# Optimization experiments

Hardware: AMD Instinct MI355X
Metric: run time of the kernel (lower is better)

## Reference

```python
import jax, jax.numpy as jnp
import numpy as np
from jax import lax

# FPN anchor layout: 800x800 image, 3 anchors/loc, strides 4,8,16,32,64
LEVEL_ANCHORS = [120000, 30000, 7500, 1875, 507]
PRE_NMS_TOP_N = 1000   # per level (test mode)
POST_NMS_TOP_N = 1000
NMS_THRESH = 0.7
MIN_SIZE = 1e-3


def setup_inputs() -> dict:
    key = jax.random.key(0)
    k1, k2, k3, k4 = jax.random.split(key, 4)
    A = sum(LEVEL_ANCHORS)
    bs = 2
    predicts = jax.random.normal(k1, (bs, A, 4), jnp.float32) * 0.1
    objectness = jax.random.normal(k2, (bs, A, 1), jnp.float32)
    cxy = jax.random.uniform(k3, (A, 2), jnp.float32, 0.0, 800.0)
    wh = jax.random.uniform(k4, (A, 2), jnp.float32, 16.0, 128.0)
    anchors = jnp.concatenate([cxy - 0.5 * wh, cxy + 0.5 * wh], axis=-1)
    valid_size = jnp.full((bs, 2), 800.0, jnp.float32)  # (w, h) per image
    return {"predicts": predicts, "objectness": objectness,
            "anchors": anchors, "valid_size": valid_size}


def _decode(predicts, anchors):
    # BoxCoder.decoder with weights [1,1,1,1]
    awh = anchors[:, 2:] - anchors[:, :2]          # [A,2]
    axy = anchors[:, :2] + 0.5 * awh               # [A,2]
    xy = axy + predicts[..., :2] * awh             # [bs,A,2] center
    wh = jnp.exp(predicts[..., 2:]) * awh          # [bs,A,2]
    x1y1 = xy - 0.5 * wh
    return jnp.concatenate([x1y1, x1y1 + wh], axis=-1)  # [bs,A,4]


def _per_level_topk_idx(scores):
    # scores: [bs, A] -> concat of per-level top-k indices (global anchor ids)
    idx_list, offset = [], 0
    for n in LEVEL_ANCHORS:
        k = min(PRE_NMS_TOP_N, n)
        _, top = lax.top_k(scores[:, offset:offset + n], k)
        idx_list.append(top + offset)
        offset += n
    return jnp.concatenate(idx_list, axis=1)  # [bs, K]


def _nms_keep(boxes, valid, thresh):
    # boxes sorted by score desc; returns boolean keep mask (sequential NMS)
    x1, y1, x2, y2 = boxes[:, 0], boxes[:, 1], boxes[:, 2], boxes[:, 3]
    area = (x2 - x1) * (y2 - y1)
    xx1 = jnp.maximum(x1[:, None], x1[None, :])
    yy1 = jnp.maximum(y1[:, None], y1[None, :])
    xx2 = jnp.minimum(x2[:, None], x2[None, :])
    yy2 = jnp.minimum(y2[:, None], y2[None, :])
    inter = jnp.maximum(xx2 - xx1, 0.0) * jnp.maximum(yy2 - yy1, 0.0)
    iou = inter / (area[:, None] + area[None, :] - inter + 1e-9)
    sup = iou > thresh                                   # [N,N]
    N = boxes.shape[0]
    ar = jnp.arange(N)

    def body(i, keep):
        suppressed = jnp.any((ar < i) & keep & sup[i])
        return keep.at[i].set(keep[i] & ~suppressed)

    return lax.fori_loop(0, N, body, valid)


def _filter_image(boxes, scores, lvls, wh):
    # boxes [K,4], scores [K], lvls [K] int, wh [2]=(w,h)
    w, h = wh[0], wh[1]
    x1 = jnp.clip(boxes[:, 0], 0.0, w)
    y1 = jnp.clip(boxes[:, 1], 0.0, h)
    x2 = jnp.clip(boxes[:, 2], 0.0, w)
    y2 = jnp.clip(boxes[:, 3], 0.0, h)
    boxes = jnp.stack([x1, y1, x2, y2], axis=-1)
    valid = (x2 - x1 > MIN_SIZE) & (y2 - y1 > MIN_SIZE)
    s = jnp.where(valid, scores, -jnp.inf)
    order = jnp.argsort(-s)
    boxes, s, lvls, valid = boxes[order], s[order], lvls[order], valid[order]
    # batched_nms: offset each level into a disjoint coordinate range
    max_coord = lax.stop_gradient(jnp.max(boxes)) + 1.0
    off = lvls.astype(boxes.dtype) * max_coord
    keep = _nms_keep(lax.stop_gradient(boxes) + off[:, None], valid, NMS_THRESH)
    # take first POST_NMS_TOP_N kept (boxes are score-sorted)
    rank = jnp.cumsum(keep) - 1
    slot = jnp.where(keep & (rank < POST_NMS_TOP_N), rank, POST_NMS_TOP_N)
    out_b = jnp.zeros((POST_NMS_TOP_N + 1, 4), boxes.dtype).at[slot].set(boxes)[:POST_NMS_TOP_N]
    out_s = jnp.zeros((POST_NMS_TOP_N + 1,), s.dtype).at[slot].set(
        jnp.where(keep, s, 0.0))[:POST_NMS_TOP_N]
    return out_b, out_s


def reference(predicts, objectness, anchors, valid_size):
    bs = predicts.shape[0]
    proposals = _decode(predicts, anchors)            # [bs,A,4]
    scores = objectness[..., 0]                       # [bs,A]
    idx = _per_level_topk_idx(scores)                 # [bs,K]
    bidx = jnp.arange(bs)[:, None]
    boxes = proposals[bidx, idx]                      # [bs,K,4]
    sc = scores[bidx, idx]                            # [bs,K]
    levels_all = jnp.concatenate(
        [jnp.full((n,), i, jnp.int32) for i, n in enumerate(LEVEL_ANCHORS)])
    lvl = levels_all[idx]                             # [bs,K]
    final_boxes, final_scores = jax.vmap(_filter_image)(boxes, sc, lvl, valid_size)
    return final_boxes, final_scores
```

## Files before the change

kernel.cpp:

```cpp
#include <hip/hip_runtime.h>

typedef unsigned int u32;
typedef unsigned long long u64;

#define A_TOT    159882
#define BS       2
#define KTOP     1000
#define CAND_CAP 4096
#define HB       4096
#define ABLK     4096
#define NBH      40
#define EPT      16

static const size_t HIST12_OFF   = 0;
static const size_t CUT_OFF      = 131072;
static const size_t CCNT_OFF     = 131104;
static const size_t MAXC_OFF     = 131136;
static const size_t NV_OFF       = 131144;
static const size_t CHUNKANY_OFF = 131200;
static const size_t ZERO_END     = 132480;
static const size_t CAND_OFF     = 132480;
static const size_t LKEY2_OFF    = 394624;
static const size_t LBOX_OFF     = 476544;
static const size_t LSC_OFF      = 640384;
static const size_t RANK_OFF     = 681344;
static const size_t MASK_OFF     = 759168;

__device__ __forceinline__ int level_of(int a) {
  if (a < 120000) return 0;
  if (a < 150000) return 1;
  if (a < 157500) return 2;
  if (a < 159375) return 3;
  return 4;
}

__device__ __forceinline__ u32 dkey(float s) {
  u32 b = __float_as_uint(s);
  return (b & 0x80000000u) ? b : (~b & 0x7FFFFFFFu);
}
__device__ __forceinline__ float dkey_inv(u32 d) {
  u32 b = (d & 0x80000000u) ? d : (~d & 0x7FFFFFFFu);
  return __uint_as_float(b);
}

__device__ __forceinline__ void decode_clip(const float* __restrict__ pred,
                                            const float* __restrict__ anch,
                                            const float* __restrict__ vs,
                                            int b, int a,
                                            float& x1c, float& y1c, float& x2c, float& y2c,
                                            bool& valid) {
  const float* pp = pred + ((size_t)b * A_TOT + (size_t)a) * 4;
  const float* aa = anch + (size_t)a * 4;
  float ax1 = aa[0], ay1 = aa[1], ax2 = aa[2], ay2 = aa[3];
  float px = pp[0], py = pp[1], pw = pp[2], ph = pp[3];
  float aw  = __fsub_rn(ax2, ax1);
  float ah  = __fsub_rn(ay2, ay1);
  float acx = __fadd_rn(ax1, __fmul_rn(0.5f, aw));
  float acy = __fadd_rn(ay1, __fmul_rn(0.5f, ah));
  float cx  = __fadd_rn(acx, __fmul_rn(px, aw));
  float cy  = __fadd_rn(acy, __fmul_rn(py, ah));
  float w   = __fmul_rn(expf(pw), aw);
  float h   = __fmul_rn(expf(ph), ah);
  float x1  = __fsub_rn(cx, __fmul_rn(0.5f, w));
  float y1  = __fsub_rn(cy, __fmul_rn(0.5f, h));
  float x2  = __fadd_rn(x1, w);
  float y2  = __fadd_rn(y1, h);
  float Wv = vs[b * 2 + 0], Hv = vs[b * 2 + 1];
  x1c = fminf(fmaxf(x1, 0.0f), Wv);
  y1c = fminf(fmaxf(y1, 0.0f), Hv);
  x2c = fminf(fmaxf(x2, 0.0f), Wv);
  y2c = fminf(fmaxf(y2, 0.0f), Hv);
  valid = (__fsub_rn(x2c, x1c) > 0.001f) && (__fsub_rn(y2c, y1c) > 0.001f);
}

__device__ __forceinline__ void bitonic_u64(u64* arr, int N, int t, int nt) {
// ... 31 lines not shown
        bool sw = up ? (a > b2) : (a < b2);
        if (sw) { v[0] = b2; v[1] = a; }
      } else if (j <= 64) {
        int dl = j >> 1;
        bool up = (((2 * tid) & k) == 0);
        bool low = ((tid & dl) == 0);
        bool keepmin = (low == up);
#pragma unroll
        for (int e = 0; e < 2; ++e) {
          u64 o = shfl_xor_u64(v[e], dl);
          v[e] = keepmin ? (v[e] < o ? v[e] : o) : (v[e] > o ? v[e] : o);
        }
      } else {
        u64* B = bufs[cur]; cur ^= 1;
        B[2 * tid] = v[0]; B[2 * tid + 1] = v[1];
        __syncthreads();
#pragma unroll
        for (int e = 0; e < 2; ++e) {
          int i = 2 * tid + e, p = i ^ j;
          u64 o = B[p];
          bool up = ((i & k) == 0);
          bool keepmin = ((i < p) == up);
          v[e] = keepmin ? (v[e] < o ? v[e] : o) : (v[e] > o ? v[e] : o);
        }
      }
    }
  }
  u64* B = bufs[cur];
  B[2 * tid] = v[0]; B[2 * tid + 1] = v[1];
  __syncthreads();
  return B;
}

__global__ void k_zero(char* __restrict__ ws) {
  size_t i = (size_t)blockIdx.x * blockDim.x + threadIdx.x;
  if (i * 4 < ZERO_END) ((u32*)ws)[i] = 0u;
}

__global__ void k_hist12(const float* __restrict__ obj, char* __restrict__ ws) {
  __shared__ u32 h[2 * HB];
  int tid = threadIdx.x;
  int b = blockIdx.x / NBH, loc = blockIdx.x % NBH;
  int start = loc * ABLK;
  int l0 = level_of(start);
  if (l0 >= 4) return;
  for (int i = tid; i < 2 * HB; i += 256) h[i] = 0u;
  __syncthreads();
  for (int it = 0; it < EPT; ++it) {
    int a = start + it * 256 + tid;
    if (a < A_TOT) {
      int l = level_of(a);
      if (l < 4) {
        u32 d = dkey(obj[(size_t)b * A_TOT + a]);
        atomicAdd(&h[(u32)(l - l0) * HB + (d >> 20)], 1u);
      }
    }
  }
  __syncthreads();
  int lend = level_of(min(start + ABLK - 1, A_TOT - 1));
  int nseg = ((l0 + 1 <= lend) && (l0 + 1 < 4)) ? 2 : 1;
  for (int s = 0; s < nseg; ++s) {
    u32* gh = (u32*)(ws + HIST12_OFF) + (size_t)(b * 4 + l0 + s) * HB;
    for (int i = tid; i < HB; i += 256) {
      u32 v = h[s * HB + i];
      if (v) atomicAdd(&gh[i], v);
    }
  }
}

__global__ void k_compactsel(const float* __restrict__ obj, char* __restrict__ ws) {
  __shared__ u32 scan[256];
  __shared__ u32 cutv[2];
  __shared__ u32 lcnt[2], gbase[2];
  int tid = threadIdx.x, lane = tid & 63;
  int b = blockIdx.x / NBH, loc = blockIdx.x % NBH;
  int start = loc * ABLK;
  int l0 = level_of(start);
  if (l0 >= 4) return;
  int lend = level_of(min(start + ABLK - 1, A_TOT - 1));
  int nseg = ((l0 + 1 <= lend) && (l0 + 1 < 4)) ? 2 : 1;
  if (tid < 2) lcnt[tid] = 0;
  for (int s = 0; s < nseg; ++s) {
    int seg = b * 4 + l0 + s;
    const u32* gh = (const u32*)(ws + HIST12_OFF) + (size_t)seg * HB;
    u32 vals[16]; u32 acc = 0;
    for (int q = 0; q < 16; ++q) { vals[q] = gh[tid * 16 + q]; acc += vals[q]; }
    __syncthreads();
    scan[tid] = acc; __syncthreads();
    for (int d = 1; d < 256; d <<= 1) {
      u32 x = (tid >= d) ? scan[tid - d] : 0u; __syncthreads();
      scan[tid] += x; __syncthreads();
    }
    u32 incl = scan[tid], prev = incl - acc;
    if (prev < KTOP && incl >= KTOP) {
      u32 run = prev; int cb = HB - 1;
      for (int q = 0; q < 16; ++q) { run += vals[q]; if (run >= KTOP) { cb = tid * 16 + q; break; } }
      cutv[s] = (u32)cb;
      ((u32*)(ws + CUT_OFF))[seg] = (u32)cb;
    }
  }
  __syncthreads();
  u32 dv[EPT], slotv[EPT], passm = 0, sim = 0;
  for (int it = 0; it < EPT; ++it) {
    int a = start + it * 256 + tid;
    bool pass = false; u32 si = 0, d = 0;
    if (a < A_TOT) {
      int l = level_of(a);
      if (l < 4) {
        si = (u32)(l - l0);
        d = dkey(obj[(size_t)b * A_TOT + a]);
        pass = (d >> 20) <= cutv[si];
      }
    }
    dv[it] = d;
    u64 mp = __ballot(pass);
    u64 m1 = __ballot(pass && si == 1);
    u64 m0 = mp & ~m1;
    u32 slot = 0;
    if (m0) {
      int ld = __builtin_ctzll(m0);
      u32 wb = 0;
      if (lane == ld) wb = atomicAdd(&lcnt[0], (u32)__popcll(m0));
      wb = __shfl(wb, ld);
      if (pass && si == 0) slot = wb + (u32)__popcll(m0 & ((1ull << lane) - 1ull));
    }
    if (m1) {
      int ld = __builtin_ctzll(m1);
      u32 wb = 0;
      if (lane == ld) wb = atomicAdd(&lcnt[1], (u32)__popcll(m1));
      wb = __shfl(wb, ld);
      if (pass && si == 1) slot = wb + (u32)__popcll(m1 & ((1ull << lane) - 1ull));
    }
    slotv[it] = slot;
    if (pass) { passm |= 1u << it; if (si) sim |= 1u << it; }
  }
  __syncthreads();
  if (tid < 2)
    gbase[tid] = lcnt[tid] ? atomicAdd((u32*)(ws + CCNT_OFF) + (b * 4 + l0 + tid), lcnt[tid]) : 0u;
  __syncthreads();
  for (int it = 0; it < EPT; ++it) {
    if ((passm >> it) & 1u) {
      int a = start + it * 256 + tid;
      u32 si = (sim >> it) & 1u;
      int seg = b * 4 + l0 + (int)si;
      u32 gslot = gbase[si] + slotv[it];
      if (gslot < CAND_CAP)
        ((u64*)(ws + CAND_OFF))[(size_t)seg * CAND_CAP + gslot] =
            ((u64)dv[it] << 32) | ((u64)(u32)a << 12) | (u64)gslot;
    }
  }
}

__global__ __launch_bounds__(1024)
void k_sortdec(const float* __restrict__ pred, const float* __restrict__ obj,
               const float* __restrict__ anch, const float* __restrict__ vs,
               char* __restrict__ ws) {
  __shared__ u64 bufAB[4096];
  __shared__ float4 dboxS[2048];
  __shared__ float dscS[2048];
  __shared__ u32 validS[2048];
  __shared__ u64 cm[16];
  u64* bufA = bufAB; u64* bufB = bufAB + 2048;
  int tid = threadIdx.x, lane = tid & 63, wv = tid >> 6;
  int P = blockIdx.x, b = P / 5, l = P % 5;
  int n;
  u64* S;
  if (l == 4) {
    n = 507;
    u64 v[2];
#pragma unroll
    for (int e = 0; e < 2; ++e) {
      int idx = 2 * tid + e;
      if (idx < 507) {
        int a = 159375 + idx;
        float sc = obj[(size_t)b * A_TOT + a];
        float x1, y1, x2, y2; bool valid;
        decode_clip(pred, anch, vs, b, a, x1, y1, x2, y2, valid);
        dboxS[idx] = make_float4(x1, y1, x2, y2);
        dscS[idx] = sc;
        validS[idx] = valid ? 1u : 0u;
        v[e] = ((u64)dkey(sc) << 32) | ((u64)(u32)a << 12) | (u64)idx;
      } else v[e] = ~0ull;
    }
// ... 39 lines not shown
    }
  }
  float m = 0.0f;
  for (int j = tid; j < n; j += 1024) {
    int slot = (int)(S[j] & 0xFFFull);
    float4 bx = dboxS[slot];
    m = fmaxf(m, fmaxf(fmaxf(bx.x, bx.y), fmaxf(bx.z, bx.w)));
  }
  for (int off = 32; off; off >>= 1) m = fmaxf(m, __shfl_xor(m, off));
  if (lane == 0) atomicMax((u32*)(ws + MAXC_OFF) + b, __float_as_uint(m));
  {
    int j = wv * 64 + lane;
    bool val = (j < n) && (validS[(int)(S[j] & 0xFFFull)] != 0u);
    u64 mask = __ballot(val);
    if (lane == 0) cm[wv] = mask;
    __syncthreads();
    int base = 0;
    for (int w2 = 0; w2 < wv; ++w2) base += __popcll(cm[w2]);
    if (val) {
      int r = base + __popcll(mask & ((1ull << lane) - 1ull));
      int slot = (int)(S[j] & 0xFFFull);
      ((u64*)(ws + LKEY2_OFF))[(size_t)P * 1024 + r] = S[j];
      ((float4*)(ws + LBOX_OFF))[(size_t)P * 1024 + r] = dboxS[slot];
      ((float*)(ws + LSC_OFF))[(size_t)P * 1024 + r] = dscS[slot];
    }
    if (tid == 0) {
      int tot = 0;
      for (int w2 = 0; w2 < 16; ++w2) tot += __popcll(cm[w2]);
      ((u32*)(ws + NV_OFF))[P] = (u32)tot;
    }
  }
}

__device__ __forceinline__ int lbound(const u64* __restrict__ arr, int n, u64 key) {
  int lo = 0, hi = n;
  while (lo < hi) { int mid = (lo + hi) >> 1; if (arr[mid] < key) lo = mid + 1; else hi = mid; }
  return lo;
}

__global__ void k_maskrank(char* __restrict__ ws) {
  __shared__ float4 boxS[1024];
  __shared__ float  areaS[1024];
  int tid = threadIdx.x, bid = blockIdx.x;
  int P = bid >> 6, rblk = bid & 63;
  int b = P / 5, l = P % 5;
  int n = (int)((const u32*)(ws + NV_OFF))[P];
  float M = __uint_as_float(((const u32*)(ws + MAXC_OFF))[b]);
  float maxc = __fadd_rn(M, 1.0f);
  float off = __fmul_rn((float)l, maxc);
  const float4* lbox = (const float4*)(ws + LBOX_OFF) + (size_t)P * 1024;
  for (int i = tid; i < n; i += 256) {
    float4 bx = lbox[i];
    bx.x = __fadd_rn(bx.x, off); bx.y = __fadd_rn(bx.y, off);
    bx.z = __fadd_rn(bx.z, off); bx.w = __fadd_rn(bx.w, off);
    boxS[i] = bx;
    areaS[i] = __fmul_rn(__fsub_rn(bx.z, bx.x), __fsub_rn(bx.w, bx.y));
  }
  {
    int e = rblk * 16 + tid;
    if (tid < 16 && e < n) {
      const u64* lkey = (const u64*)(ws + LKEY2_OFF);
      const u32* nvp = (const u32*)(ws + NV_OFF);
      u64 key = lkey[(size_t)P * 1024 + e];
      const u64* base[4];
      int lo[4], hi[4], q2 = 0;
      for (int l2 = 0; l2 < 5; ++l2) {
        if (l2 == l) continue;
        base[q2] = lkey + (size_t)(b * 5 + l2) * 1024;
        lo[q2] = 0; hi[q2] = (int)nvp[b * 5 + l2];
        ++q2;
      }
      for (int step = 0; step < 11; ++step) {
#pragma unroll
        for (int q = 0; q < 4; ++q) {
          if (lo[q] < hi[q]) {
            int mid = (lo[q] + hi[q]) >> 1;
            u64 v = base[q][mid];
            if (v < key) lo[q] = mid + 1; else hi[q] = mid;
          }
        }
      }
      ((u32*)(ws + RANK_OFF))[(size_t)P * 1024 + e] =
          (u32)(e + lo[0] + lo[1] + lo[2] + lo[3]);
    }
  }
  __syncthreads();
  int i = rblk * 16 + (tid >> 4);
  int w = tid & 15;
  int W = (n + 63) >> 6;
  if (i >= n || w >= W) return;
  float4 bi = boxS[i];
  float ai = areaS[i];
  u64 word = 0;
  int j0 = w << 6;
  int jn = min(64, n - j0);
  if (jn == 64) {
#pragma unroll 4
    for (int t2 = 0; t2 < 64; ++t2) {
      int jj = (t2 + w) & 63;
      float4 bj = boxS[j0 + jj];
      float xx1 = fmaxf(bi.x, bj.x);
      float yy1 = fmaxf(bi.y, bj.y);
      float xx2 = fminf(bi.z, bj.z);
      float yy2 = fminf(bi.w, bj.w);
      float iw = fmaxf(__fsub_rn(xx2, xx1), 0.0f);
      float ih = fmaxf(__fsub_rn(yy2, yy1), 0.0f);
      float inter = __fmul_rn(iw, ih);
      float den = __fadd_rn(__fsub_rn(__fadd_rn(ai, areaS[j0 + jj]), inter), 1e-9f);
      float iou = __fdiv_rn(inter, den);
      if (iou > 0.7f) word |= (1ull << jj);
    }
  } else {
    for (int jj = 0; jj < jn; ++jj) {
      float4 bj = boxS[j0 + jj];
      float xx1 = fmaxf(bi.x, bj.x);
      float yy1 = fmaxf(bi.y, bj.y);
      float xx2 = fminf(bi.z, bj.z);
      float yy2 = fminf(bi.w, bj.w);
      float iw = fmaxf(__fsub_rn(xx2, xx1), 0.0f);
      float ih = fmaxf(__fsub_rn(yy2, yy1), 0.0f);
      float inter = __fmul_rn(iw, ih);
      float den = __fadd_rn(__fsub_rn(__fadd_rn(ai, areaS[j0 + jj]), inter), 1e-9f);
      float iou = __fdiv_rn(inter, den);
      if (iou > 0.7f) word |= (1ull << jj);
    }
  }
  if (i >= j0 && i < j0 + 64) word &= ~(1ull << (i - j0));
  ((u64*)(ws + MASK_OFF))[(size_t)P * 16000 + (size_t)i * W + w] = word;
  if (word)
    atomicOr((u64*)(ws + CHUNKANY_OFF) + (size_t)P * 16 + (i >> 6), 1ull << (i & 63));
}

__global__ __launch_bounds__(320)
void k_scanfin(float* __restrict__ out, char* __restrict__ ws) {
  __shared__ u64 keeps[5][16];
  __shared__ u64 kb[80];
  __shared__ u32 sb[128];
  __shared__ u32 pfx[80];
  __shared__ u32 nvs[5];
  int tid = threadIdx.x, w = tid >> 6, lane = tid & 63;
  int b = blockIdx.x;
  for (int i = tid; i < 80; i += 320) kb[i] = 0ull;
  for (int i = tid; i < 4000; i += 320) out[(size_t)b * 4000 + i] = 0.0f;
  for (int i = tid; i < 1000; i += 320) out[8000 + (size_t)b * 1000 + i] = 0.0f;
  if (tid < 5) nvs[tid] = ((const u32*)(ws + NV_OFF))[b * 5 + tid];

  int P = b * 5 + w;
  int n = (int)((const u32*)(ws + NV_OFF))[P];
  int W = (n + 63) >> 6;
  const u64* maskg = (const u64*)(ws + MASK_OFF) + (size_t)P * 16000;
  u64 ca = (lane < 16) ? ((const u64*)(ws + CHUNKANY_OFF))[(size_t)P * 16 + lane] : 0ull;
  u64 dpre[16];
#pragma unroll
  for (int c = 0; c < 16; ++c) {
    int row = (c << 6) + lane;
    dpre[c] = (c < W && row < n) ? maskg[(size_t)row * W + c] : 0ull;
  }
  u64 removed = 0ull, keepw = 0ull;
#pragma unroll
  for (int c = 0; c < 16; ++c) {
    if (c >= W) break;
    int rb = c << 6;
    int rows = min(64, n - rb);
    u64 rowsmask = (rows == 64) ? ~0ull : ((1ull << rows) - 1ull);
    u64 curw = __shfl(removed, c);
    u64 cand = ~curw & rowsmask;
    u64 ca_c = __shfl(ca, c);
    u64 keptbits;
    u64 anyrows = ca_c & cand;
    if (anyrows == 0ull) {
      keptbits = cand;
    } else {
      u64 diag = dpre[c];
      u64 diagnz = __ballot(diag != 0ull) & cand;
      if (diagnz == 0ull) {
        keptbits = cand;
      } else {
        u64 remw = curw | ~rowsmask;
        u64 kept = 0ull;
        int pos = 0;
        u64 work = diagnz;
        while (work) {
          int s = __builtin_ctzll(work); work &= work - 1;
          u64 range = (1ull << s) - (1ull << pos);
          kept |= ~remw & range;
          bool k = ((remw >> s) & 1ull) == 0ull;
          u64 dr = __shfl(diag, s);
          if (k) { kept |= 1ull << s; remw |= dr; }
          pos = s + 1;
        }
        u64 tail = (pos >= 64) ? 0ull : (~0ull << pos);
        kept |= ~remw & tail & rowsmask;
        keptbits = kept;
      }
      u64 todo = keptbits & ca_c;
      while (todo) {
        int r0 = __builtin_ctzll(todo); todo &= todo - 1;
        int r1 = -1, r2 = -1, r3 = -1;
        if (todo) { r1 = __builtin_ctzll(todo); todo &= todo - 1; }
        if (todo) { r2 = __builtin_ctzll(todo); todo &= todo - 1; }
        if (todo) { r3 = __builtin_ctzll(todo); todo &= todo - 1; }
        u64 v0 = 0, v1 = 0, v2 = 0, v3 = 0;
        if (lane < W) {
          v0 = maskg[(size_t)(rb + r0) * W + lane];
          if (r1 >= 0) v1 = maskg[(size_t)(rb + r1) * W + lane];
          if (r2 >= 0) v2 = maskg[(size_t)(rb + r2) * W + lane];
          if (r3 >= 0) v3 = maskg[(size_t)(rb + r3) * W + lane];
        }
        removed |= v0 | v1 | v2 | v3;
      }
    }
    if (lane == c) keepw |= keptbits;
  }
  if (lane < 16) keeps[w][lane] = keepw;
  __syncthreads();

  const u32* rank = (const u32*)(ws + RANK_OFF);
  for (int idx = tid; idx < 5120; idx += 320) {
    int p = idx >> 10, i = idx & 1023;
    if (i < (int)nvs[p] && ((keeps[p][i >> 6] >> (i & 63)) & 1ull)) {
      u32 r = rank[(size_t)(b * 5 + p) * 1024 + i];
      atomicOr(&kb[r >> 6], 1ull << (r & 63));
    }
  }
  __syncthreads();
  if (tid < 128) sb[tid] = (tid < 80) ? (u32)__popcll(kb[tid]) : 0u;
  __syncthreads();
  for (int d = 1; d < 128; d <<= 1) {
    u32 x = (tid < 128 && tid >= d) ? sb[tid - d] : 0u;
    __syncthreads();
    if (tid < 128) sb[tid] += x;
    __syncthreads();
  }
  if (tid < 80) pfx[tid] = sb[tid] - (u32)__popcll(kb[tid]);
  __syncthreads();
  for (int idx = tid; idx < 5120; idx += 320) {
    int p = idx >> 10, i = idx & 1023;
    if (i < (int)nvs[p] && ((keeps[p][i >> 6] >> (i & 63)) & 1ull)) {
      int Pp = b * 5 + p;
      u32 r = rank[(size_t)Pp * 1024 + i];
      u64 word = kb[r >> 6];
      int slot = (int)pfx[r >> 6] + __popcll(word & ((1ull << (r & 63)) - 1ull));
      if (slot < KTOP) {
        float4 bx = ((const float4*)(ws + LBOX_OFF))[(size_t)Pp * 1024 + i];
        float s = ((const float*)(ws + LSC_OFF))[(size_t)Pp * 1024 + i];
        float* ob = out + ((size_t)b * KTOP + slot) * 4;
        ob[0] = bx.x; ob[1] = bx.y; ob[2] = bx.z; ob[3] = bx.w;
        out[8000 + (size_t)b * KTOP + slot] = s;
      }
    }
  }
}

extern "C" void kernel_launch(void* const* d_in, const int* in_sizes, int n_in,
                              void* d_out, int out_size, void* d_ws, size_t ws_size,
                              hipStream_t stream) {
  const float* pred = (const float*)d_in[0];
  const float* obj  = (const float*)d_in[1];
  const float* anch = (const float*)d_in[2];
  const float* vs   = (const float*)d_in[3];
  float* out = (float*)d_out;
  char* ws = (char*)d_ws;
  (void)in_sizes; (void)n_in; (void)out_size; (void)ws_size;

  int gZ = (int)((ZERO_END / 4 + 255) / 256);
  k_zero      <<<gZ,        256, 0, stream>>>(ws);
  k_hist12    <<<BS * NBH,  256, 0, stream>>>(obj, ws);
  k_compactsel<<<BS * NBH,  256, 0, stream>>>(obj, ws);
  k_sortdec   <<<10,       1024, 0, stream>>>(pred, obj, anch, vs, ws);
  k_maskrank  <<<640,       256, 0, stream>>>(ws);
  k_scanfin   <<<2,         320, 0, stream>>>(out, ws);
}
```

Before: 164.3 us.

## Fuse histogram/compaction and mask/scan kernels with software grid barriers

Merges the histogram and compaction kernels into one kernel, which caches the score keys in shared memory and uses a spin-wait grid barrier in global memory. It also merges the IoU mask/rank kernel with the final NMS scan kernel through a second grid barrier, so only two blocks continue to the sequential scan. This removes two kernel launches and a second read of the objectness scores. The cost is added spin-wait barriers, which need every block to be resident at once (640 blocks of 320 threads), and agent-scope atomic loads and stores that may be slower than plain memory accesses.

Result: slower. 232.1 us (+41.2%).

```diff
diff --git a/kernel.cpp b/kernel.cpp
--- a/kernel.cpp
+++ b/kernel.cpp
@@ -13,10 +13,10 @@
 #define EPT      16
 
 static const size_t HIST12_OFF   = 0;
-static const size_t CUT_OFF      = 131072;
 static const size_t CCNT_OFF     = 131104;
 static const size_t MAXC_OFF     = 131136;
 static const size_t NV_OFF       = 131144;
+static const size_t BAR_OFF      = 131184;
 static const size_t CHUNKANY_OFF = 131200;
 static const size_t ZERO_END     = 132480;
 static const size_t CAND_OFF     = 132480;
@@ -41,6 +41,30 @@
 __device__ __forceinline__ float dkey_inv(u32 d) {
   u32 b = (d & 0x80000000u) ? d : (~d & 0x7FFFFFFFu);
   return __uint_as_float(b);
+}
+
+__device__ __forceinline__ u64 ld_agent_u64(const u64* p) {
+  return __hip_atomic_load(p, __ATOMIC_RELAXED, __HIP_MEMORY_SCOPE_AGENT);
+}
+__device__ __forceinline__ u32 ld_agent_u32(const u32* p) {
+  return __hip_atomic_load(p, __ATOMIC_RELAXED, __HIP_MEMORY_SCOPE_AGENT);
+}
+__device__ __forceinline__ void st_agent_u64(u64* p, u64 v) {
+  __hip_atomic_store(p, v, __ATOMIC_RELAXED, __HIP_MEMORY_SCOPE_AGENT);
+}
+__device__ __forceinline__ void st_agent_u32(u32* p, u32 v) {
+  __hip_atomic_store(p, v, __ATOMIC_RELAXED, __HIP_MEMORY_SCOPE_AGENT);
+}
+
+__device__ __forceinline__ void grid_barrier(u32* cnt, u32 nblk, bool fence) {
+  __syncthreads();
+  if (threadIdx.x == 0) {
+    if (fence) __threadfence();
+    __hip_atomic_fetch_add(cnt, 1u, __ATOMIC_ACQ_REL, __HIP_MEMORY_SCOPE_AGENT);
+    while (__hip_atomic_load(cnt, __ATOMIC_ACQUIRE, __HIP_MEMORY_SCOPE_AGENT) < nblk)
+      __builtin_amdgcn_s_sleep(2);
+  }
+  __syncthreads();
 }
 
 __device__ __forceinline__ void decode_clip(const float* __restrict__ pred,
@@ -143,38 +167,10 @@
   if (i * 4 < ZERO_END) ((u32*)ws)[i] = 0u;
 }
 
-__global__ void k_hist12(const float* __restrict__ obj, char* __restrict__ ws) {
+__global__ __launch_bounds__(256)
+void k_histcompact(const float* __restrict__ obj, char* __restrict__ ws) {
   __shared__ u32 h[2 * HB];
-  int tid = threadIdx.x;
-  int b = blockIdx.x / NBH, loc = blockIdx.x % NBH;
-  int start = loc * ABLK;
-  int l0 = level_of(start);
-  if (l0 >= 4) return;
-  for (int i = tid; i < 2 * HB; i += 256) h[i] = 0u;
-  __syncthreads();
-  for (int it = 0; it < EPT; ++it) {
-    int a = start + it * 256 + tid;
-    if (a < A_TOT) {
-      int l = level_of(a);
-      if (l < 4) {
-        u32 d = dkey(obj[(size_t)b * A_TOT + a]);
-        atomicAdd(&h[(u32)(l - l0) * HB + (d >> 20)], 1u);
-      }
-    }
-  }
-  __syncthreads();
-  int lend = level_of(min(start + ABLK - 1, A_TOT - 1));
-  int nseg = ((l0 + 1 <= lend) && (l0 + 1 < 4)) ? 2 : 1;
-  for (int s = 0; s < nseg; ++s) {
-    u32* gh = (u32*)(ws + HIST12_OFF) + (size_t)(b * 4 + l0 + s) * HB;
-    for (int i = tid; i < HB; i += 256) {
-      u32 v = h[s * HB + i];
-      if (v) atomicAdd(&gh[i], v);
-    }
-  }
-}
-
-__global__ void k_compactsel(const float* __restrict__ obj, char* __restrict__ ws) {
+  __shared__ u32 dk[ABLK];
   __shared__ u32 scan[256];
   __shared__ u32 cutv[2];
   __shared__ u32 lcnt[2], gbase[2];
@@ -182,15 +178,44 @@
   int b = blockIdx.x / NBH, loc = blockIdx.x % NBH;
   int start = loc * ABLK;
   int l0 = level_of(start);
-  if (l0 >= 4) return;
-  int lend = level_of(min(start + ABLK - 1, A_TOT - 1));
-  int nseg = ((l0 + 1 <= lend) && (l0 + 1 < 4)) ? 2 : 1;
+  bool active = (l0 < 4);
+  int nseg = 0;
+  if (active) {
+    int lend = level_of(min(start + ABLK - 1, A_TOT - 1));
+    nseg = ((l0 + 1 <= lend) && (l0 + 1 < 4)) ? 2 : 1;
+    for (int i = tid; i < 2 * HB; i += 256) h[i] = 0u;
+    __syncthreads();
+    for (int it = 0; it < EPT; ++it) {
+      int a = start + it * 256 + tid;
+      u32 d = 0;
+      if (a < A_TOT) {
+        d = dkey(obj[(size_t)b * A_TOT + a]);
+        int l = level_of(a);
+        if (l < 4) atomicAdd(&h[(u32)(l - l0) * HB + (d >> 20)], 1u);
+      }
+      dk[it * 256 + tid] = d;
+    }
+    __syncthreads();
+    for (int s = 0; s < nseg; ++s) {
+      u32* gh = (u32*)(ws + HIST12_OFF) + (size_t)(b * 4 + l0 + s) * HB;
+      for (int i = tid; i < HB; i += 256) {
+        u32 v = h[s * HB + i];
+        if (v) atomicAdd(&gh[i], v);
+      }
+    }
+  }
+  grid_barrier((u32*)(ws + BAR_OFF), (u32)(BS * NBH), false);
+  if (!active) return;
+
   if (tid < 2) lcnt[tid] = 0;
   for (int s = 0; s < nseg; ++s) {
     int seg = b * 4 + l0 + s;
     const u32* gh = (const u32*)(ws + HIST12_OFF) + (size_t)seg * HB;
     u32 vals[16]; u32 acc = 0;
-    for (int q = 0; q < 16; ++q) { vals[q] = gh[tid * 16 + q]; acc += vals[q]; }
+    for (int q = 0; q < 16; ++q) {
+      vals[q] = ld_agent_u32(&gh[tid * 16 + q]);
+      acc += vals[q];
+    }
     __syncthreads();
     scan[tid] = acc; __syncthreads();
     for (int d = 1; d < 256; d <<= 1) {
@@ -202,23 +227,21 @@
       u32 run = prev; int cb = HB - 1;
       for (int q = 0; q < 16; ++q) { run += vals[q]; if (run >= KTOP) { cb = tid * 16 + q; break; } }
       cutv[s] = (u32)cb;
-      ((u32*)(ws + CUT_OFF))[seg] = (u32)cb;
-    }
-  }
-  __syncthreads();
-  u32 dv[EPT], slotv[EPT], passm = 0, sim = 0;
+    }
+  }
+  __syncthreads();
+  u32 slotv[EPT], passm = 0, sim = 0;
   for (int it = 0; it < EPT; ++it) {
     int a = start + it * 256 + tid;
-    bool pass = false; u32 si = 0, d = 0;
+    bool pass = false; u32 si = 0;
+    u32 d = dk[it * 256 + tid];
     if (a < A_TOT) {
       int l = level_of(a);
       if (l < 4) {
         si = (u32)(l - l0);
-        d = dkey(obj[(size_t)b * A_TOT + a]);
         pass = (d >> 20) <= cutv[si];
       }
     }
-    dv[it] = d;
     u64 mp = __ballot(pass);
     u64 m1 = __ballot(pass && si == 1);
     u64 m0 = mp & ~m1;
@@ -252,7 +275,7 @@
       u32 gslot = gbase[si] + slotv[it];
       if (gslot < CAND_CAP)
         ((u64*)(ws + CAND_OFF))[(size_t)seg * CAND_CAP + gslot] =
-            ((u64)dv[it] << 32) | ((u64)(u32)a << 12) | (u64)gslot;
+            ((u64)dk[it * 256 + tid] << 32) | ((u64)(u32)a << 12) | (u64)gslot;
     }
   }
 }
@@ -360,114 +383,116 @@
   }
 }
 
-__device__ __forceinline__ int lbound(const u64* __restrict__ arr, int n, u64 key) {
-  int lo = 0, hi = n;
-  while (lo < hi) { int mid = (lo + hi) >> 1; if (arr[mid] < key) lo = mid + 1; else hi = mid; }
-  return lo;
-}
-
-__global__ void k_maskrank(char* __restrict__ ws) {
+__global__ __launch_bounds__(320, 4)
+void k_maskscan(float* __restrict__ out, char* __restrict__ ws) {
   __shared__ float4 boxS[1024];
   __shared__ float  areaS[1024];
-  int tid = threadIdx.x, bid = blockIdx.x;
-  int P = bid >> 6, rblk = bid & 63;
-  int b = P / 5, l = P % 5;
-  int n = (int)((const u32*)(ws + NV_OFF))[P];
-  float M = __uint_as_float(((const u32*)(ws + MAXC_OFF))[b]);
-  float maxc = __fadd_rn(M, 1.0f);
-  float off = __fmul_rn((float)l, maxc);
-  const float4* lbox = (const float4*)(ws + LBOX_OFF) + (size_t)P * 1024;
-  for (int i = tid; i < n; i += 256) {
-    float4 bx = lbox[i];
-    bx.x = __fadd_rn(bx.x, off); bx.y = __fadd_rn(bx.y, off);
-    bx.z = __fadd_rn(bx.z, off); bx.w = __fadd_rn(bx.w, off);
-    boxS[i] = bx;
-    areaS[i] = __fmul_rn(__fsub_rn(bx.z, bx.x), __fsub_rn(bx.w, bx.y));
-  }
-  {
-    int e = rblk * 16 + tid;
-    if (tid < 16 && e < n) {
-      const u64* lkey = (const u64*)(ws + LKEY2_OFF);
-      const u32* nvp = (const u32*)(ws + NV_OFF);
-      u64 key = lkey[(size_t)P * 1024 + e];
-      const u64* base[4];
-      int lo[4], hi[4], q2 = 0;
-      for (int l2 = 0; l2 < 5; ++l2) {
-        if (l2 == l) continue;
-        base[q2] = lkey + (size_t)(b * 5 + l2) * 1024;
-        lo[q2] = 0; hi[q2] = (int)nvp[b * 5 + l2];
-        ++q2;
-      }
-      for (int step = 0; step < 11; ++step) {
-#pragma unroll
-        for (int q = 0; q < 4; ++q) {
-          if (lo[q] < hi[q]) {
-            int mid = (lo[q] + hi[q]) >> 1;
-            u64 v = base[q][mid];
-            if (v < key) lo[q] = mid + 1; else hi[q] = mid;
-          }
-        }
-      }
-      ((u32*)(ws + RANK_OFF))[(size_t)P * 1024 + e] =
-          (u32)(e + lo[0] + lo[1] + lo[2] + lo[3]);
-    }
-  }
-  __syncthreads();
-  int i = rblk * 16 + (tid >> 4);
-  int w = tid & 15;
-  int W = (n + 63) >> 6;
-  if (i >= n || w >= W) return;
-  float4 bi = boxS[i];
-  float ai = areaS[i];
-  u64 word = 0;
-  int j0 = w << 6;
-  int jn = min(64, n - j0);
-  if (jn == 64) {
-#pragma unroll 4
-    for (int t2 = 0; t2 < 64; ++t2) {
-      int jj = (t2 + w) & 63;
-      float4 bj = boxS[j0 + jj];
-      float xx1 = fmaxf(bi.x, bj.x);
-      float yy1 = fmaxf(bi.y, bj.y);
-      float xx2 = fminf(bi.z, bj.z);
-      float yy2 = fminf(bi.w, bj.w);
-      float iw = fmaxf(__fsub_rn(xx2, xx1), 0.0f);
-      float ih = fmaxf(__fsub_rn(yy2, yy1), 0.0f);
-      float inter = __fmul_rn(iw, ih);
-      float den = __fadd_rn(__fsub_rn(__fadd_rn(ai, areaS[j0 + jj]), inter), 1e-9f);
-      float iou = __fdiv_rn(inter, den);
-      if (iou > 0.7f) word |= (1ull << jj);
-    }
-  } else {
-    for (int jj = 0; jj < jn; ++jj) {
-      float4 bj = boxS[j0 + jj];
-      float xx1 = fmaxf(bi.x, bj.x);
-      float yy1 = fmaxf(bi.y, bj.y);
-      float xx2 = fminf(bi.z, bj.z);
-      float yy2 = fminf(bi.w, bj.w);
-      float iw = fmaxf(__fsub_rn(xx2, xx1), 0.0f);
-      float ih = fmaxf(__fsub_rn(yy2, yy1), 0.0f);
-      float inter = __fmul_rn(iw, ih);
-      float den = __fadd_rn(__fsub_rn(__fadd_rn(ai, areaS[j0 + jj]), inter), 1e-9f);
-      float iou = __fdiv_rn(inter, den);
-      if (iou > 0.7f) word |= (1ull << jj);
-    }
-  }
-  if (i >= j0 && i < j0 + 64) word &= ~(1ull << (i - j0));
-  ((u64*)(ws + MASK_OFF))[(size_t)P * 16000 + (size_t)i * W + w] = word;
-  if (word)
-    atomicOr((u64*)(ws + CHUNKANY_OFF) + (size_t)P * 16 + (i >> 6), 1ull << (i & 63));
-}
-
-__global__ __launch_bounds__(320)
-void k_scanfin(float* __restrict__ out, char* __restrict__ ws) {
   __shared__ u64 keeps[5][16];
   __shared__ u64 kb[80];
   __shared__ u32 sb[128];
   __shared__ u32 pfx[80];
   __shared__ u32 nvs[5];
-  int tid = threadIdx.x, w = tid >> 6, lane = tid & 63;
-  int b = blockIdx.x;
+  int tid = threadIdx.x;
+  int bid = blockIdx.x;
+
+  {
+    int P = bid >> 6, rblk = bid & 63;
+    int b = P / 5, l = P % 5;
+    int n = (int)((const u32*)(ws + NV_OFF))[P];
+    float M = __uint_as_float(((const u32*)(ws + MAXC_OFF))[b]);
+    float maxc = __fadd_rn(M, 1.0f);
+    float off = __fmul_rn((float)l, maxc);
+    const float4* lbox = (const float4*)(ws + LBOX_OFF) + (size_t)P * 1024;
+    for (int i = tid; i < n; i += 320) {
+      float4 bx = lbox[i];
+      bx.x = __fadd_rn(bx.x, off); bx.y = __fadd_rn(bx.y, off);
+      bx.z = __fadd_rn(bx.z, off); bx.w = __fadd_rn(bx.w, off);
+      boxS[i] = bx;
+      areaS[i] = __fmul_rn(__fsub_rn(bx.z, bx.x), __fsub_rn(bx.w, bx.y));
+    }
+    {
+      int e = rblk * 16 + tid;
+      if (tid < 16 && e < n) {
+        const u64* lkey = (const u64*)(ws + LKEY2_OFF);
+        const u32* nvp = (const u32*)(ws + NV_OFF);
+        u64 key = lkey[(size_t)P * 1024 + e];
+        const u64* base[4];
+        int lo[4], hi[4], q2 = 0;
+        for (int l2 = 0; l2 < 5; ++l2) {
+          if (l2 == l) continue;
+          base[q2] = lkey + (size_t)(b * 5 + l2) * 1024;
+          lo[q2] = 0; hi[q2] = (int)nvp[b * 5 + l2];
+          ++q2;
+        }
+        for (int step = 0; step < 11; ++step) {
+#pragma unroll
+          for (int q = 0; q < 4; ++q) {
+            if (lo[q] < hi[q]) {
+              int mid = (lo[q] + hi[q]) >> 1;
+              u64 v = base[q][mid];
+              if (v < key) lo[q] = mid + 1; else hi[q] = mid;
+            }
+          }
+        }
+        st_agent_u32((u32*)(ws + RANK_OFF) + (size_t)P * 1024 + e,
+                     (u32)(e + lo[0] + lo[1] + lo[2] + lo[3]));
+      }
+    }
+    __syncthreads();
+    if (tid < 256) {
+      int i = rblk * 16 + (tid >> 4);
+      int w = tid & 15;
+      int W = (n + 63) >> 6;
+      if (i < n && w < W) {
+        float4 bi = boxS[i];
+        float ai = areaS[i];
+        u64 word = 0;
+        int j0 = w << 6;
+        int jn = min(64, n - j0);
+        if (jn == 64) {
+#pragma unroll 4
+          for (int t2 = 0; t2 < 64; ++t2) {
+            int jj = (t2 + w) & 63;
+            float4 bj = boxS[j0 + jj];
+            float xx1 = fmaxf(bi.x, bj.x);
+            float yy1 = fmaxf(bi.y, bj.y);
+            float xx2 = fminf(bi.z, bj.z);
+            float yy2 = fminf(bi.w, bj.w);
+            float iw = fmaxf(__fsub_rn(xx2, xx1), 0.0f);
+            float ih = fmaxf(__fsub_rn(yy2, yy1), 0.0f);
+            float inter = __fmul_rn(iw, ih);
+            float den = __fadd_rn(__fsub_rn(__fadd_rn(ai, areaS[j0 + jj]), inter), 1e-9f);
+            float iou = __fdiv_rn(inter, den);
+            if (iou > 0.7f) word |= (1ull << jj);
+          }
+        } else {
+          for (int jj = 0; jj < jn; ++jj) {
+            float4 bj = boxS[j0 + jj];
+            float xx1 = fmaxf(bi.x, bj.x);
+            float yy1 = fmaxf(bi.y, bj.y);
+            float xx2 = fminf(bi.z, bj.z);
+            float yy2 = fminf(bi.w, bj.w);
+            float iw = fmaxf(__fsub_rn(xx2, xx1), 0.0f);
+            float ih = fmaxf(__fsub_rn(yy2, yy1), 0.0f);
+            float inter = __fmul_rn(iw, ih);
+            float den = __fadd_rn(__fsub_rn(__fadd_rn(ai, areaS[j0 + jj]), inter), 1e-9f);
+            float iou = __fdiv_rn(inter, den);
+            if (iou > 0.7f) word |= (1ull << jj);
+          }
+        }
+        if (i >= j0 && i < j0 + 64) word &= ~(1ull << (i - j0));
+        st_agent_u64((u64*)(ws + MASK_OFF) + (size_t)P * 16000 + (size_t)i * W + w, word);
+        if (word)
+          atomicOr((u64*)(ws + CHUNKANY_OFF) + (size_t)P * 16 + (i >> 6), 1ull << (i & 63));
+      }
+    }
+  }
+
+  grid_barrier((u32*)(ws + BAR_OFF) + 1, (u32)(BS * 5 * 64), true);
+  if (bid >= BS) return;
+
+  int w = tid >> 6, lane = tid & 63;
+  int b = bid;
   for (int i = tid; i < 80; i += 320) kb[i] = 0ull;
   for (int i = tid; i < 4000; i += 320) out[(size_t)b * 4000 + i] = 0.0f;
   for (int i = tid; i < 1000; i += 320) out[8000 + (size_t)b * 1000 + i] = 0.0f;
@@ -477,12 +502,13 @@
   int n = (int)((const u32*)(ws + NV_OFF))[P];
   int W = (n + 63) >> 6;
   const u64* maskg = (const u64*)(ws + MASK_OFF) + (size_t)P * 16000;
-  u64 ca = (lane < 16) ? ((const u64*)(ws + CHUNKANY_OFF))[(size_t)P * 16 + lane] : 0ull;
+  u64 ca = (lane < 16) ? ld_agent_u64((const u64*)(ws + CHUNKANY_OFF) + (size_t)P * 16 + lane)
+                       : 0ull;
   u64 dpre[16];
 #pragma unroll
   for (int c = 0; c < 16; ++c) {
     int row = (c << 6) + lane;
-    dpre[c] = (c < W && row < n) ? maskg[(size_t)row * W + c] : 0ull;
+    dpre[c] = (c < W && row < n) ? ld_agent_u64(&maskg[(size_t)row * W + c]) : 0ull;
   }
   u64 removed = 0ull, keepw = 0ull;
 #pragma unroll
@@ -530,10 +556,10 @@
         if (todo) { r3 = __builtin_ctzll(todo); todo &= todo - 1; }
         u64 v0 = 0, v1 = 0, v2 = 0, v3 = 0;
         if (lane < W) {
-          v0 = maskg[(size_t)(rb + r0) * W + lane];
-          if (r1 >= 0) v1 = maskg[(size_t)(rb + r1) * W + lane];
-          if (r2 >= 0) v2 = maskg[(size_t)(rb + r2) * W + lane];
-          if (r3 >= 0) v3 = maskg[(size_t)(rb + r3) * W + lane];
+          v0 = ld_agent_u64(&maskg[(size_t)(rb + r0) * W + lane]);
+          if (r1 >= 0) v1 = ld_agent_u64(&maskg[(size_t)(rb + r1) * W + lane]);
+          if (r2 >= 0) v2 = ld_agent_u64(&maskg[(size_t)(rb + r2) * W + lane]);
+          if (r3 >= 0) v3 = ld_agent_u64(&maskg[(size_t)(rb + r3) * W + lane]);
         }
         removed |= v0 | v1 | v2 | v3;
       }
@@ -547,7 +573,7 @@
   for (int idx = tid; idx < 5120; idx += 320) {
     int p = idx >> 10, i = idx & 1023;
     if (i < (int)nvs[p] && ((keeps[p][i >> 6] >> (i & 63)) & 1ull)) {
-      u32 r = rank[(size_t)(b * 5 + p) * 1024 + i];
+      u32 r = ld_agent_u32(&rank[(size_t)(b * 5 + p) * 1024 + i]);
       atomicOr(&kb[r >> 6], 1ull << (r & 63));
     }
   }
@@ -566,7 +592,7 @@
     int p = idx >> 10, i = idx & 1023;
     if (i < (int)nvs[p] && ((keeps[p][i >> 6] >> (i & 63)) & 1ull)) {
       int Pp = b * 5 + p;
-      u32 r = rank[(size_t)Pp * 1024 + i];
+      u32 r = ld_agent_u32(&rank[(size_t)Pp * 1024 + i]);
       u64 word = kb[r >> 6];
       int slot = (int)pfx[r >> 6] + __popcll(word & ((1ull << (r & 63)) - 1ull));
       if (slot < KTOP) {
@@ -592,10 +618,8 @@
   (void)in_sizes; (void)n_in; (void)out_size; (void)ws_size;
 
   int gZ = (int)((ZERO_END / 4 + 255) / 256);
-  k_zero      <<<gZ,        256, 0, stream>>>(ws);
-  k_hist12    <<<BS * NBH,  256, 0, stream>>>(obj, ws);
-  k_compactsel<<<BS * NBH,  256, 0, stream>>>(obj, ws);
-  k_sortdec   <<<10,       1024, 0, stream>>>(pred, obj, anch, vs, ws);
-  k_maskrank  <<<640,       256, 0, stream>>>(ws);
-  k_scanfin   <<<2,         320, 0, stream>>>(out, ws);
-}
+  k_zero       <<<gZ,       256, 0, stream>>>(ws);
+  k_histcompact<<<BS * NBH, 256, 0, stream>>>(obj, ws);
+  k_sortdec    <<<10,      1024, 0, stream>>>(pred, obj, anch, vs, ws);
+  k_maskscan   <<<BS * 5 * 64, 320, 0, stream>>>(out, ws);
+}
```

## Fuse histogram and compaction kernels with a software grid barrier

Applied to the files above, without the earlier changes.

Merges the histogram kernel and the candidate-compaction kernel into one launch, with an atomic-counter grid barrier in between so every block sees the complete global histogram. Each block keeps its objectness keys in shared memory across the barrier instead of reading them from global memory a second time. This removes one kernel launch and a redundant global read. In exchange it depends on all 80 blocks being resident at once, which holds on this GPU, and it drops the write of the cutoff values to the workspace.

After: 167.2 us. About the same (+1.8%).

```diff
diff --git a/kernel.cpp b/kernel.cpp
--- a/kernel.cpp
+++ b/kernel.cpp
@@ -13,10 +13,10 @@
 #define EPT      16
 
 static const size_t HIST12_OFF   = 0;
-static const size_t CUT_OFF      = 131072;
 static const size_t CCNT_OFF     = 131104;
 static const size_t MAXC_OFF     = 131136;
 static const size_t NV_OFF       = 131144;
+static const size_t BAR_OFF      = 131184;
 static const size_t CHUNKANY_OFF = 131200;
 static const size_t ZERO_END     = 132480;
 static const size_t CAND_OFF     = 132480;
@@ -41,6 +41,21 @@
 __device__ __forceinline__ float dkey_inv(u32 d) {
   u32 b = (d & 0x80000000u) ? d : (~d & 0x7FFFFFFFu);
   return __uint_as_float(b);
+}
+
+__device__ __forceinline__ u32 ld_agent_u32(const u32* p) {
+  return __hip_atomic_load(p, __ATOMIC_RELAXED, __HIP_MEMORY_SCOPE_AGENT);
+}
+
+__device__ __forceinline__ void grid_barrier(u32* cnt, u32 nblk, bool fence) {
+  __syncthreads();
+  if (threadIdx.x == 0) {
+    if (fence) __threadfence();
+    __hip_atomic_fetch_add(cnt, 1u, __ATOMIC_ACQ_REL, __HIP_MEMORY_SCOPE_AGENT);
+    while (__hip_atomic_load(cnt, __ATOMIC_ACQUIRE, __HIP_MEMORY_SCOPE_AGENT) < nblk)
+      __builtin_amdgcn_s_sleep(2);
+  }
+  __syncthreads();
 }
 
 __device__ __forceinline__ void decode_clip(const float* __restrict__ pred,
@@ -143,38 +158,10 @@
   if (i * 4 < ZERO_END) ((u32*)ws)[i] = 0u;
 }
 
-__global__ void k_hist12(const float* __restrict__ obj, char* __restrict__ ws) {
+__global__ __launch_bounds__(256)
+void k_histcompact(const float* __restrict__ obj, char* __restrict__ ws) {
   __shared__ u32 h[2 * HB];
-  int tid = threadIdx.x;
-  int b = blockIdx.x / NBH, loc = blockIdx.x % NBH;
-  int start = loc * ABLK;
-  int l0 = level_of(start);
-  if (l0 >= 4) return;
-  for (int i = tid; i < 2 * HB; i += 256) h[i] = 0u;
-  __syncthreads();
-  for (int it = 0; it < EPT; ++it) {
-    int a = start + it * 256 + tid;
-    if (a < A_TOT) {
-      int l = level_of(a);
-      if (l < 4) {
-        u32 d = dkey(obj[(size_t)b * A_TOT + a]);
-        atomicAdd(&h[(u32)(l - l0) * HB + (d >> 20)], 1u);
-      }
-    }
-  }
-  __syncthreads();
-  int lend = level_of(min(start + ABLK - 1, A_TOT - 1));
-  int nseg = ((l0 + 1 <= lend) && (l0 + 1 < 4)) ? 2 : 1;
-  for (int s = 0; s < nseg; ++s) {
-    u32* gh = (u32*)(ws + HIST12_OFF) + (size_t)(b * 4 + l0 + s) * HB;
-    for (int i = tid; i < HB; i += 256) {
-      u32 v = h[s * HB + i];
-      if (v) atomicAdd(&gh[i], v);
-    }
-  }
-}
-
-__global__ void k_compactsel(const float* __restrict__ obj, char* __restrict__ ws) {
+  __shared__ u32 dk[ABLK];
   __shared__ u32 scan[256];
   __shared__ u32 cutv[2];
   __shared__ u32 lcnt[2], gbase[2];
@@ -182,15 +169,44 @@
   int b = blockIdx.x / NBH, loc = blockIdx.x % NBH;
   int start = loc * ABLK;
   int l0 = level_of(start);
-  if (l0 >= 4) return;
-  int lend = level_of(min(start + ABLK - 1, A_TOT - 1));
-  int nseg = ((l0 + 1 <= lend) && (l0 + 1 < 4)) ? 2 : 1;
+  bool active = (l0 < 4);
+  int nseg = 0;
+  if (active) {
+    int lend = level_of(min(start + ABLK - 1, A_TOT - 1));
+    nseg = ((l0 + 1 <= lend) && (l0 + 1 < 4)) ? 2 : 1;
+    for (int i = tid; i < 2 * HB; i += 256) h[i] = 0u;
+    __syncthreads();
+    for (int it = 0; it < EPT; ++it) {
+      int a = start + it * 256 + tid;
+      u32 d = 0;
+      if (a < A_TOT) {
+        d = dkey(obj[(size_t)b * A_TOT + a]);
+        int l = level_of(a);
+        if (l < 4) atomicAdd(&h[(u32)(l - l0) * HB + (d >> 20)], 1u);
+      }
+      dk[it * 256 + tid] = d;
+    }
+    __syncthreads();
+    for (int s = 0; s < nseg; ++s) {
+      u32* gh = (u32*)(ws + HIST12_OFF) + (size_t)(b * 4 + l0 + s) * HB;
+      for (int i = tid; i < HB; i += 256) {
+        u32 v = h[s * HB + i];
+        if (v) atomicAdd(&gh[i], v);
+      }
+    }
+  }
+  grid_barrier((u32*)(ws + BAR_OFF), (u32)(BS * NBH), false);
+  if (!active) return;
+
   if (tid < 2) lcnt[tid] = 0;
   for (int s = 0; s < nseg; ++s) {
     int seg = b * 4 + l0 + s;
     const u32* gh = (const u32*)(ws + HIST12_OFF) + (size_t)seg * HB;
     u32 vals[16]; u32 acc = 0;
-    for (int q = 0; q < 16; ++q) { vals[q] = gh[tid * 16 + q]; acc += vals[q]; }
+    for (int q = 0; q < 16; ++q) {
+      vals[q] = ld_agent_u32(&gh[tid * 16 + q]);
+      acc += vals[q];
+    }
     __syncthreads();
     scan[tid] = acc; __syncthreads();
     for (int d = 1; d < 256; d <<= 1) {
@@ -202,23 +218,21 @@
       u32 run = prev; int cb = HB - 1;
       for (int q = 0; q < 16; ++q) { run += vals[q]; if (run >= KTOP) { cb = tid * 16 + q; break; } }
       cutv[s] = (u32)cb;
-      ((u32*)(ws + CUT_OFF))[seg] = (u32)cb;
-    }
-  }
-  __syncthreads();
-  u32 dv[EPT], slotv[EPT], passm = 0, sim = 0;
+    }
+  }
+  __syncthreads();
+  u32 slotv[EPT], passm = 0, sim = 0;
   for (int it = 0; it < EPT; ++it) {
     int a = start + it * 256 + tid;
-    bool pass = false; u32 si = 0, d = 0;
+    bool pass = false; u32 si = 0;
+    u32 d = dk[it * 256 + tid];
     if (a < A_TOT) {
       int l = level_of(a);
       if (l < 4) {
         si = (u32)(l - l0);
-        d = dkey(obj[(size_t)b * A_TOT + a]);
         pass = (d >> 20) <= cutv[si];
       }
     }
-    dv[it] = d;
     u64 mp = __ballot(pass);
     u64 m1 = __ballot(pass && si == 1);
     u64 m0 = mp & ~m1;
@@ -252,7 +266,7 @@
       u32 gslot = gbase[si] + slotv[it];
       if (gslot < CAND_CAP)
         ((u64*)(ws + CAND_OFF))[(size_t)seg * CAND_CAP + gslot] =
-            ((u64)dv[it] << 32) | ((u64)(u32)a << 12) | (u64)gslot;
+            ((u64)dk[it * 256 + tid] << 32) | ((u64)(u32)a << 12) | (u64)gslot;
     }
   }
 }
@@ -592,10 +606,9 @@
   (void)in_sizes; (void)n_in; (void)out_size; (void)ws_size;
 
   int gZ = (int)((ZERO_END / 4 + 255) / 256);
-  k_zero      <<<gZ,        256, 0, stream>>>(ws);
-  k_hist12    <<<BS * NBH,  256, 0, stream>>>(obj, ws);
-  k_compactsel<<<BS * NBH,  256, 0, stream>>>(obj, ws);
-  k_sortdec   <<<10,       1024, 0, stream>>>(pred, obj, anch, vs, ws);
-  k_maskrank  <<<640,       256, 0, stream>>>(ws);
-  k_scanfin   <<<2,         320, 0, stream>>>(out, ws);
-}
+  k_zero       <<<gZ,        256, 0, stream>>>(ws);
+  k_histcompact<<<BS * NBH,  256, 0, stream>>>(obj, ws);
+  k_sortdec    <<<10,       1024, 0, stream>>>(pred, obj, anch, vs, ws);
+  k_maskrank   <<<640,       256, 0, stream>>>(ws);
+  k_scanfin    <<<2,         320, 0, stream>>>(out, ws);
+}
```

## Fuse histogram and candidate compaction into one per-level select kernel

Applied to the files above, without the earlier changes.

Replaces the zero, global-histogram and compaction kernels with a single kernel per (image, level) that builds the radix histogram in shared memory, finds the top-k cutoff bin, and compacts candidates with a shared atomic counter. Zeroing shrinks to a memset of the counter region only. The mask kernel also skips words below the diagonal, so only the upper-triangular suppression mask is computed. This removes launches and global atomics, but uses just 8 blocks, so the level-0 segment of 120k elements is scanned by a single block, which limits parallelism.

Result: slower. 209.6 us (+27.5%).

```diff
diff --git a/kernel.cpp b/kernel.cpp
--- a/kernel.cpp
+++ b/kernel.cpp
@@ -8,12 +8,7 @@
 #define KTOP     1000
 #define CAND_CAP 4096
 #define HB       4096
-#define ABLK     4096
-#define NBH      40
-#define EPT      16
-
-static const size_t HIST12_OFF   = 0;
-static const size_t CUT_OFF      = 131072;
+
 static const size_t CCNT_OFF     = 131104;
 static const size_t MAXC_OFF     = 131136;
 static const size_t NV_OFF       = 131144;
@@ -138,123 +133,58 @@
   return B;
 }
 
-__global__ void k_zero(char* __restrict__ ws) {
-  size_t i = (size_t)blockIdx.x * blockDim.x + threadIdx.x;
-  if (i * 4 < ZERO_END) ((u32*)ws)[i] = 0u;
-}
-
-__global__ void k_hist12(const float* __restrict__ obj, char* __restrict__ ws) {
-  __shared__ u32 h[2 * HB];
+__global__ __launch_bounds__(1024)
+void k_select(const float* __restrict__ obj, char* __restrict__ ws) {
+  __shared__ u32 h[2][HB];
+  __shared__ u32 partial[1024];
+  __shared__ u32 cutS, cntS;
   int tid = threadIdx.x;
-  int b = blockIdx.x / NBH, loc = blockIdx.x % NBH;
-  int start = loc * ABLK;
-  int l0 = level_of(start);
-  if (l0 >= 4) return;
-  for (int i = tid; i < 2 * HB; i += 256) h[i] = 0u;
-  __syncthreads();
-  for (int it = 0; it < EPT; ++it) {
-    int a = start + it * 256 + tid;
-    if (a < A_TOT) {
-      int l = level_of(a);
-      if (l < 4) {
-        u32 d = dkey(obj[(size_t)b * A_TOT + a]);
-        atomicAdd(&h[(u32)(l - l0) * HB + (d >> 20)], 1u);
-      }
-    }
-  }
-  __syncthreads();
-  int lend = level_of(min(start + ABLK - 1, A_TOT - 1));
-  int nseg = ((l0 + 1 <= lend) && (l0 + 1 < 4)) ? 2 : 1;
-  for (int s = 0; s < nseg; ++s) {
-    u32* gh = (u32*)(ws + HIST12_OFF) + (size_t)(b * 4 + l0 + s) * HB;
-    for (int i = tid; i < HB; i += 256) {
-      u32 v = h[s * HB + i];
-      if (v) atomicAdd(&gh[i], v);
-    }
-  }
-}
-
-__global__ void k_compactsel(const float* __restrict__ obj, char* __restrict__ ws) {
-  __shared__ u32 scan[256];
-  __shared__ u32 cutv[2];
-  __shared__ u32 lcnt[2], gbase[2];
-  int tid = threadIdx.x, lane = tid & 63;
-  int b = blockIdx.x / NBH, loc = blockIdx.x % NBH;
-  int start = loc * ABLK;
-  int l0 = level_of(start);
-  if (l0 >= 4) return;
-  int lend = level_of(min(start + ABLK - 1, A_TOT - 1));
-  int nseg = ((l0 + 1 <= lend) && (l0 + 1 < 4)) ? 2 : 1;
-  if (tid < 2) lcnt[tid] = 0;
-  for (int s = 0; s < nseg; ++s) {
-    int seg = b * 4 + l0 + s;
-    const u32* gh = (const u32*)(ws + HIST12_OFF) + (size_t)seg * HB;
-    u32 vals[16]; u32 acc = 0;
-    for (int q = 0; q < 16; ++q) { vals[q] = gh[tid * 16 + q]; acc += vals[q]; }
+  int sb = blockIdx.x;
+  int b = sb >> 2, l = sb & 3;
+  const int starts[5] = {0, 120000, 150000, 157500, 159375};
+  int base = starts[l], len = starts[l + 1] - base;
+  for (int i = tid; i < 2 * HB; i += 1024) h[i >> 12][i & (HB - 1)] = 0u;
+  if (tid == 0) { cntS = 0u; cutS = HB - 1; }
+  __syncthreads();
+  const float* op = obj + (size_t)b * A_TOT + base;
+  int rep = (tid >> 6) & 1;
+  for (int i = tid; i < len; i += 1024)
+    atomicAdd(&h[rep][dkey(op[i]) >> 20], 1u);
+  __syncthreads();
+  u32 v0 = h[0][4 * tid]     + h[1][4 * tid];
+  u32 v1 = h[0][4 * tid + 1] + h[1][4 * tid + 1];
+  u32 v2 = h[0][4 * tid + 2] + h[1][4 * tid + 2];
+  u32 v3 = h[0][4 * tid + 3] + h[1][4 * tid + 3];
+  u32 acc = v0 + v1 + v2 + v3;
+  partial[tid] = acc;
+  __syncthreads();
+  for (int d = 1; d < 1024; d <<= 1) {
+    u32 x = (tid >= d) ? partial[tid - d] : 0u;
     __syncthreads();
-    scan[tid] = acc; __syncthreads();
-    for (int d = 1; d < 256; d <<= 1) {
-      u32 x = (tid >= d) ? scan[tid - d] : 0u; __syncthreads();
-      scan[tid] += x; __syncthreads();
-    }
-    u32 incl = scan[tid], prev = incl - acc;
-    if (prev < KTOP && incl >= KTOP) {
-      u32 run = prev; int cb = HB - 1;
-      for (int q = 0; q < 16; ++q) { run += vals[q]; if (run >= KTOP) { cb = tid * 16 + q; break; } }
-      cutv[s] = (u32)cb;
-      ((u32*)(ws + CUT_OFF))[seg] = (u32)cb;
-    }
-  }
-  __syncthreads();
-  u32 dv[EPT], slotv[EPT], passm = 0, sim = 0;
-  for (int it = 0; it < EPT; ++it) {
-    int a = start + it * 256 + tid;
-    bool pass = false; u32 si = 0, d = 0;
-    if (a < A_TOT) {
-      int l = level_of(a);
-      if (l < 4) {
-        si = (u32)(l - l0);
-        d = dkey(obj[(size_t)b * A_TOT + a]);
-        pass = (d >> 20) <= cutv[si];
-      }
-    }
-    dv[it] = d;
-    u64 mp = __ballot(pass);
-    u64 m1 = __ballot(pass && si == 1);
-    u64 m0 = mp & ~m1;
-    u32 slot = 0;
-    if (m0) {
-      int ld = __builtin_ctzll(m0);
-      u32 wb = 0;
-      if (lane == ld) wb = atomicAdd(&lcnt[0], (u32)__popcll(m0));
-      wb = __shfl(wb, ld);
-      if (pass && si == 0) slot = wb + (u32)__popcll(m0 & ((1ull << lane) - 1ull));
-    }
-    if (m1) {
-      int ld = __builtin_ctzll(m1);
-      u32 wb = 0;
-      if (lane == ld) wb = atomicAdd(&lcnt[1], (u32)__popcll(m1));
-      wb = __shfl(wb, ld);
-      if (pass && si == 1) slot = wb + (u32)__popcll(m1 & ((1ull << lane) - 1ull));
-    }
-    slotv[it] = slot;
-    if (pass) { passm |= 1u << it; if (si) sim |= 1u << it; }
-  }
-  __syncthreads();
-  if (tid < 2)
-    gbase[tid] = lcnt[tid] ? atomicAdd((u32*)(ws + CCNT_OFF) + (b * 4 + l0 + tid), lcnt[tid]) : 0u;
-  __syncthreads();
-  for (int it = 0; it < EPT; ++it) {
-    if ((passm >> it) & 1u) {
-      int a = start + it * 256 + tid;
-      u32 si = (sim >> it) & 1u;
-      int seg = b * 4 + l0 + (int)si;
-      u32 gslot = gbase[si] + slotv[it];
-      if (gslot < CAND_CAP)
-        ((u64*)(ws + CAND_OFF))[(size_t)seg * CAND_CAP + gslot] =
-            ((u64)dv[it] << 32) | ((u64)(u32)a << 12) | (u64)gslot;
-    }
-  }
+    partial[tid] += x;
+    __syncthreads();
+  }
+  u32 incl = partial[tid], prev = incl - acc;
+  if (prev < KTOP && incl >= KTOP) {
+    u32 run = prev, cb = 4 * tid + 3;
+    if ((run + v0) >= KTOP) cb = 4 * tid;
+    else if ((run + v0 + v1) >= KTOP) cb = 4 * tid + 1;
+    else if ((run + v0 + v1 + v2) >= KTOP) cb = 4 * tid + 2;
+    cutS = cb;
+  }
+  __syncthreads();
+  u32 cut = cutS;
+  u64* cand = (u64*)(ws + CAND_OFF) + (size_t)(b * 4 + l) * CAND_CAP;
+  for (int i = tid; i < len; i += 1024) {
+    u32 d = dkey(op[i]);
+    if ((d >> 20) <= cut) {
+      u32 s = atomicAdd(&cntS, 1u);
+      if (s < CAND_CAP)
+        cand[s] = ((u64)d << 32) | ((u64)(u32)(base + i) << 12) | (u64)(s & 0xFFFu);
+    }
+  }
+  __syncthreads();
+  if (tid == 0) ((u32*)(ws + CCNT_OFF))[b * 4 + l] = cntS;
 }
 
 __global__ __launch_bounds__(1024)
@@ -360,12 +290,6 @@
   }
 }
 
-__device__ __forceinline__ int lbound(const u64* __restrict__ arr, int n, u64 key) {
-  int lo = 0, hi = n;
-  while (lo < hi) { int mid = (lo + hi) >> 1; if (arr[mid] < key) lo = mid + 1; else hi = mid; }
-  return lo;
-}
-
 __global__ void k_maskrank(char* __restrict__ ws) {
   __shared__ float4 boxS[1024];
   __shared__ float  areaS[1024];
@@ -416,7 +340,7 @@
   int i = rblk * 16 + (tid >> 4);
   int w = tid & 15;
   int W = (n + 63) >> 6;
-  if (i >= n || w >= W) return;
+  if (i >= n || w >= W || w < (i >> 6)) return;
   float4 bi = boxS[i];
   float ai = areaS[i];
   u64 word = 0;
@@ -591,11 +515,9 @@
   char* ws = (char*)d_ws;
   (void)in_sizes; (void)n_in; (void)out_size; (void)ws_size;
 
-  int gZ = (int)((ZERO_END / 4 + 255) / 256);
-  k_zero      <<<gZ,        256, 0, stream>>>(ws);
-  k_hist12    <<<BS * NBH,  256, 0, stream>>>(obj, ws);
-  k_compactsel<<<BS * NBH,  256, 0, stream>>>(obj, ws);
-  k_sortdec   <<<10,       1024, 0, stream>>>(pred, obj, anch, vs, ws);
-  k_maskrank  <<<640,       256, 0, stream>>>(ws);
-  k_scanfin   <<<2,         320, 0, stream>>>(out, ws);
-}
+  hipMemsetAsync(ws + CCNT_OFF, 0, ZERO_END - CCNT_OFF, stream);
+  k_select  <<<BS * 4,  1024, 0, stream>>>(obj, ws);
+  k_sortdec <<<10,      1024, 0, stream>>>(pred, obj, anch, vs, ws);
+  k_maskrank<<<640,      256, 0, stream>>>(ws);
+  k_scanfin <<<2,        320, 0, stream>>>(out, ws);
+}
```
